# Kernel optimization log

Measured on AMD Instinct MI355X. Metric: run time of the kernel, lower is better.

Reference implementation:

```python
import jax, jax.numpy as jnp
import numpy as np

T, N, D = 64, 40, 4
H, R, K = 256, 64, 2
E = N * (N - 1)


def _xavier(key, shape):
    std = (2.0 / (shape[0] + shape[1])) ** 0.5
    return (std * jax.random.normal(key, shape)).astype(jnp.float32)


def setup_inputs() -> dict:
    ks = iter(jax.random.split(jax.random.key(0), 40))
    send, recv = np.where(np.ones((N, N)) - np.eye(N))  # fully-connected directed graph, E = N*(N-1)
    p = {}
    p['inputs'] = jax.random.normal(next(ks), (1, T, N, D), dtype=jnp.float32)
    p['node_masks'] = jnp.ones((1, T, N), dtype=jnp.float32)
    p['send_edges'] = jnp.asarray(send, dtype=jnp.int32)
    p['recv_edges'] = jnp.asarray(recv, dtype=jnp.int32)
    for name, nin in (('mlp1', D), ('mlp2', 2 * H), ('mlp3', H), ('mlp4', 3 * H)):
        p[name + '_W1'] = _xavier(next(ks), (H, nin))
        p[name + '_b1'] = jnp.full((H,), 0.1, jnp.float32)
        p[name + '_W2'] = _xavier(next(ks), (H, H))
        p[name + '_b2'] = jnp.full((H,), 0.1, jnp.float32)
    s = float(1.0 / np.sqrt(R))
    for nm in ('fwd', 'rev'):
        p[nm + '_Wih'] = jax.random.uniform(next(ks), (4 * R, H), jnp.float32, -s, s)
        p[nm + '_Whh'] = jax.random.uniform(next(ks), (4 * R, R), jnp.float32, -s, s)
        p[nm + '_bih'] = jnp.zeros((4 * R,), jnp.float32)
        p[nm + '_bhh'] = jnp.zeros((4 * R,), jnp.float32)
    p['enc_W'] = _xavier(next(ks), (K, 2 * R))
    p['enc_b'] = jnp.full((K,), 0.1, jnp.float32)
    p['prior_W'] = _xavier(next(ks), (K, R))
    p['prior_b'] = jnp.full((K,), 0.1, jnp.float32)
    return p


def _mlp(x, W1, b1, W2, b2):
    # RefNRIMLP in eval mode with no_bn=True: elu(fc2(elu(fc1(x))))
    return jax.nn.elu(jax.nn.elu(x @ W1.T + b1) @ W2.T + b2)


def _lstm(xs, Wih, Whh, bih, bhh):
    # xs: [T, E, H] -> hidden states [T, E, R]; PyTorch LSTM gate order i, f, g, o
    def step(carry, xt):
        h, c = carry
        g = xt @ Wih.T + bih + h @ Whh.T + bhh
        i, f, gg, o = jnp.split(g, 4, axis=-1)
        c = jax.nn.sigmoid(f) * c + jax.nn.sigmoid(i) * jnp.tanh(gg)
        h = jax.nn.sigmoid(o) * jnp.tanh(c)
        return (h, c), h
    Rh = Whh.shape[1]
    init = (jnp.zeros((xs.shape[1], Rh), xs.dtype), jnp.zeros((xs.shape[1], Rh), xs.dtype))
    _, hs = jax.lax.scan(step, init, xs)
    return hs


def _encode(inputs, send, recv,
            m1W1, m1b1, m1W2, m1b2, m2W1, m2b1, m2W2, m2b2,
            m3W1, m3b1, m3W2, m3b2, m4W1, m4b1, m4W2, m4b2,
            fWih, fWhh, fbih, fbhh, rWih, rWhh, rbih, rbhh,
            encW, encb, priW, prib):
    x = inputs[0]                                                  # [T, N, D]
    h = _mlp(x, m1W1, m1b1, m1W2, m1b2)                            # [T, N, H]
    e = jnp.concatenate([h[:, send], h[:, recv]], axis=-1)         # node2edge gather [T, E, 2H]
    e = _mlp(e, m2W1, m2b1, m2W2, m2b2)                            # [T, E, H]
    skip = e
    n = jnp.zeros((x.shape[0], x.shape[1], e.shape[-1]), e.dtype)
    n = n.at[:, recv].add(e)                                       # edge2node scatter-add (index_add_)
    n = _mlp(n, m3W1, m3b1, m3W2, m3b2)                            # [T, N, H]
    e = jnp.concatenate([n[:, send], n[:, recv], skip], axis=-1)   # [T, E, 3H]
    e = _mlp(e, m4W1, m4b1, m4W2, m4b2)                            # per-edge features over time [T, E, H]
    fwd_h = _lstm(e, fWih, fWhh, fbih, fbhh)                       # [T, E, R]
    rev_h = _lstm(e[::-1], rWih, rWhh, rbih, rbhh)[::-1]           # [T, E, R]
    prior = fwd_h @ priW.T + prib                                  # [T, E, K]
    enc = jnp.concatenate([fwd_h, rev_h], axis=-1) @ encW.T + encb # [T, E, K]
    return jnp.concatenate([prior, enc], axis=-1)                  # [T, E, 2K]


def reference(inputs, node_masks, send_edges, recv_edges,
              mlp1_W1, mlp1_b1, mlp1_W2, mlp1_b2,
              mlp2_W1, mlp2_b1, mlp2_W2, mlp2_b2,
              mlp3_W1, mlp3_b1, mlp3_W2, mlp3_b2,
              mlp4_W1, mlp4_b1, mlp4_W2, mlp4_b2,
              fwd_Wih, fwd_Whh, fwd_bih, fwd_bhh,
              rev_Wih, rev_Whh, rev_bih, rev_bhh,
              enc_W, enc_b, prior_W, prior_b):
    del node_masks  # all nodes present -> static fully-connected graph each step
    return _encode(inputs, send_edges, recv_edges,
                   mlp1_W1, mlp1_b1, mlp1_W2, mlp1_b2,
                   mlp2_W1, mlp2_b1, mlp2_W2, mlp2_b2,
                   mlp3_W1, mlp3_b1, mlp3_W2, mlp3_b2,
                   mlp4_W1, mlp4_b1, mlp4_W2, mlp4_b2,
                   fwd_Wih, fwd_Whh, fwd_bih, fwd_bhh,
                   rev_Wih, rev_Whh, rev_bih, rev_bhh,
                   enc_W, enc_b, prior_W, prior_b)
```

## Files before the change

### kernel.cpp

```cpp
#include <hip/hip_runtime.h>
#include <math.h>

#define T_ 64
#define N_ 40
#define D_ 4
#define H_ 256
#define R_ 64
#define E_ 1560
#define TE_ (T_*E_)
#define TN_ (T_*N_)

typedef unsigned short us;
typedef short short8 __attribute__((ext_vector_type(8)));
typedef float f32x4 __attribute__((ext_vector_type(4)));

__device__ __forceinline__ float elu_f(float x){ return x > 0.f ? x : (__expf(x) - 1.f); }
__device__ __forceinline__ float sig_f(float x){ return 1.f/(1.f+__expf(-x)); }
__device__ __forceinline__ float tanh_f(float x){ return 2.f/(1.f+__expf(-2.f*x)) - 1.f; }
__device__ __forceinline__ float dot4(float4 a, float4 b){ return a.x*b.x + a.y*b.y + a.z*b.z + a.w*b.w; }

__device__ __forceinline__ float bf2f(us u){ return __uint_as_float(((unsigned int)u) << 16); }
__device__ __forceinline__ us f2bf(float f){
    unsigned int u = __float_as_uint(f);
    u += 0x7FFFu + ((u >> 16) & 1u);
    return (us)(u >> 16);
}
__device__ __forceinline__ float4 ld4f(const float* p){ return *(const float4*)p; }
__device__ __forceinline__ float4 ld4f(const us* p){
    ushort4 v = *(const ushort4*)p;
    return make_float4(bf2f(v.x), bf2f(v.y), bf2f(v.z), bf2f(v.w));
}
__device__ __forceinline__ void st4f(float* p, float4 v){ *(float4*)p = v; }
__device__ __forceinline__ void st4f(us* p, float4 v){
    ushort4 o; o.x = f2bf(v.x); o.y = f2bf(v.y); o.z = f2bf(v.z); o.w = f2bf(v.w);
    *(ushort4*)p = o;
}

__device__ __forceinline__ void gld16(void* lds, const void* g){
    __builtin_amdgcn_global_load_lds((const __attribute__((address_space(1))) unsigned int*)g,
                                     (__attribute__((address_space(3))) unsigned int*)lds,
                                     16, 0, 0);
}

__device__ __forceinline__ void wsplit1(const float* W, us* hi, us* lo, int i){
    const float w = W[i];
    const us h = f2bf(w);
    hi[i] = h;
    lo[i] = f2bf(w - bf2f(h));
}

__device__ __forceinline__ void wsplitF(const float* __restrict__ W, int stride, int colOff,
                                        us* hi, us* lo, int i){
    const int jj   = i & 7;
    const int lane = (i >> 3) & 63;
    const int mt   = (i >> 9) & 1;
    const int k    = (i >> 10) & 7;
    const int fh   = i >> 13;
    const int R = fh * 32 + mt * 16 + (lane & 15);
    const int K = k * 32 + (lane >> 4) * 8 + jj;
    const float w = W[(size_t)R * stride + colOff + K];
    const us h = f2bf(w);
    hi[i] = h;
    lo[i] = f2bf(w - bf2f(h));
}

__global__ __launch_bounds__(256)
void wsplit_all(const float* __restrict__ s0, us* h0, us* l0,
                const float* __restrict__ s1, us* h1, us* l1,
                const float* __restrict__ s2, us* h2, us* l2,
                const float* __restrict__ s3, us* h3, us* l3,
                const float* __restrict__ s4, us* h4, us* l4,
                const float* __restrict__ s5, us* h5, us* l5,
                const float* __restrict__ s6, us* h6, us* l6)
{
    int i = blockIdx.x * 256 + threadIdx.x;
    if (i < 65536) { wsplitF(s0, 256,   0, h0, l0, i); return; } i -= 65536;
    if (i < 65536) { wsplitF(s1, 768, 512, h1, l1, i); return; } i -= 65536;
    if (i < 65536) { wsplitF(s2, 256,   0, h2, l2, i); return; } i -= 65536;
    if (i < 65536) { wsplitF(s3, 256,   0, h3, l3, i); return; } i -= 65536;
    if (i < 65536) { wsplitF(s4, 256,   0, h4, l4, i); return; } i -= 65536;
    if (i < 16384) { wsplit1(s5, h5, l5, i); return; } i -= 16384;
    wsplit1(s6, h6, l6, i);
}

__global__ __launch_bounds__(256)
void mlp1_kernel(const float* __restrict__ x,
                 const float* __restrict__ W1, const float* __restrict__ b1,
                 const float* __restrict__ W2, const float* __restrict__ b2,
                 us* __restrict__ hout)
{
    __shared__ float xs[8][4];
    __shared__ float h1[8][256];
    const int tid = threadIdx.x;
    const int r0  = blockIdx.x * 8;

    if (tid < 32) xs[tid >> 2][tid & 3] = x[r0 * 4 + tid];
    __syncthreads();

    const float4 w1 = *(const float4*)&W1[tid * 4];
    const float bb1 = b1[tid];
    #pragma unroll
    for (int row = 0; row < 8; ++row) {
        float v = bb1 + xs[row][0]*w1.x + xs[row][1]*w1.y + xs[row][2]*w1.z + xs[row][3]*w1.w;
        h1[row][tid] = elu_f(v);
    }
    __syncthreads();

    float acc[8];
    const float bb2 = b2[tid];
    #pragma unroll
    for (int row = 0; row < 8; ++row) acc[row] = bb2;
    const float* w2row = W2 + (size_t)tid * 256;
    for (int k4 = 0; k4 < 64; ++k4) {
        const float4 w = *(const float4*)&w2row[k4 * 4];
        #pragma unroll
        for (int row = 0; row < 8; ++row) {
            const float4 hh = *(const float4*)&h1[row][k4 * 4];
            acc[row] += dot4(hh, w);
        }
    }
    #pragma unroll
    for (int row = 0; row < 8; ++row)
        hout[(size_t)(r0 + row) * 256 + tid] = f2bf(elu_f(acc[row]));
}

__global__ __launch_bounds__(256)
void node_proj(const us* __restrict__ A, const float* __restrict__ W,
               int wstride, float* __restrict__ P)
{
    __shared__ float As[16][64];
    __shared__ float Ws[16][64];

    const int tid  = threadIdx.x;
    const int am   = tid >> 2;
    const int gm   = blockIdx.x * 64 + am;
    const int part = blockIdx.y >> 2;
    const int wq   = blockIdx.y & 3;

    const us* aptr = A + (size_t)gm * 256;
    const float* wptr = W + (size_t)(wq * 64 + am) * wstride + part * 256;

    const int tx = tid & 15, ty = tid >> 4;
    float acc[4][4] = {};

    for (int k0 = 0; k0 < 256; k0 += 16) {
        const float4 a4 = ld4f(aptr + k0 + (tid & 3) * 4);
        const float4 w4 = *(const float4*)(wptr + k0 + (tid & 3) * 4);

        __syncthreads();
        const int ak = (tid & 3) * 4;
        As[ak+0][am] = a4.x; As[ak+1][am] = a4.y; As[ak+2][am] = a4.z; As[ak+3][am] = a4.w;
        Ws[ak+0][am] = w4.x; Ws[ak+1][am] = w4.y; Ws[ak+2][am] = w4.z; Ws[ak+3][am] = w4.w;
        __syncthreads();

        #pragma unroll
        for (int kq = 0; kq < 16; ++kq) {
            const float4 av = *(const float4*)&As[kq][ty * 4];
            const float4 wv = *(const float4*)&Ws[kq][tx * 4];
            const float a_[4] = {av.x, av.y, av.z, av.w};
            const float w_[4] = {wv.x, wv.y, wv.z, wv.w};
            #pragma unroll
            for (int i = 0; i < 4; ++i)
                #pragma unroll
                for (int j = 0; j < 4; ++j)
                    acc[i][j] += a_[i] * w_[j];
        }
    }

    const int gn = part * 256 + wq * 64 + tx * 4;
    #pragma unroll
    for (int i = 0; i < 4; ++i) {
        const int row = blockIdx.x * 64 + ty * 4 + i;
        float4 o;
        o.x = acc[i][0]; o.y = acc[i][1]; o.z = acc[i][2]; o.w = acc[i][3];
        *(float4*)(P + (size_t)row * 512 + gn) = o;
    }
}

#define VM0   0x3F70

#define GEMM_CORE64(WHp, WLp)                                                            \
    {                                                                                    \
        const us* wbh = (WHp) + w * 8192 + lane * 8;                                     \
        const us* wbl = (WLp) + w * 8192 + lane * 8;                                     \
        _Pragma("unroll")                                                                \
        for (int k = 0; k < 8; ++k) {                                                    \
            short8 wh[2], wl[2], ef[4];                                                  \
            _Pragma("unroll")                                                            \
            for (int mt = 0; mt < 2; ++mt) {                                             \
                wh[mt] = *(const short8*)(wbh + (k * 2 + mt) * 512);                     \
                wl[mt] = *(const short8*)(wbl + (k * 2 + mt) * 512);                     \
            }                                                                            \
            _Pragma("unroll")                                                            \
            for (int nt = 0; nt < 4; ++nt)                                               \
                ef[nt] = *(const short8*)(AG + k * 4096 + nt * 1024 + ml * 64 + qs16);   \
            __builtin_amdgcn_s_setprio(1);                                               \
            _Pragma("unroll")                                                            \
            for (int nt = 0; nt < 4; ++nt)                                               \
                _Pragma("unroll")                                                        \
                for (int mt = 0; mt < 2; ++mt) {                                         \
                    acc[mt][nt] = __builtin_amdgcn_mfma_f32_16x16x32_bf16(               \
                        wh[mt], ef[nt], acc[mt][nt], 0, 0, 0);                           \
                    acc[mt][nt] = __builtin_amdgcn_mfma_f32_16x16x32_bf16(               \
                        wl[mt], ef[nt], acc[mt][nt], 0, 0, 0);                           \
                }                                                                        \
            __builtin_amdgcn_s_setprio(0);                                               \
        }                                                                                \
    }

__global__ __launch_bounds__(512, 4)
void gemm_bf(const float* __restrict__ Ptab, const float* __restrict__ b1,
             const int* __restrict__ send, const int* __restrict__ recv,
             const us* __restrict__ WH, const us* __restrict__ WL,
             const float* __restrict__ bias2, us* __restrict__ C)
{
    __shared__ char AG[32768];

    const int tid = threadIdx.x, lane = tid & 63, w = tid >> 6;
    const int ml = lane & 15, q = lane >> 4;
    const int qs16 = (q ^ ((ml >> 1) & 3)) * 16;
    const int bx = blockIdx.x;

    {
        int srw[4], rrw[4];
        #pragma unroll
        for (int nt = 0; nt < 4; ++nt) {
            const int row = bx * 64 + nt * 16 + ml;
            const int t = row / E_;
            const int e = row - t * E_;
            srw[nt] = t * N_ + send[e];
            rrw[nt] = t * N_ + recv[e];
        }
        #pragma unroll
        for (int mt = 0; mt < 2; ++mt) {
            const int col = w * 32 + mt * 16 + q * 4;
            const float4 bb = *(const float4*)(b1 + col);
            const int of = w * 4096 + ml * 64 + (((mt * 2 + (q >> 1)) ^ ((ml >> 1) & 3)) * 16) + (q & 1) * 8;
            #pragma unroll
            for (int nt = 0; nt < 4; ++nt) {
                const float4 a = *(const float4*)(Ptab + (size_t)srw[nt] * 512 + col);
                const float4 b = *(const float4*)(Ptab + (size_t)rrw[nt] * 512 + 256 + col);
                float4 v;
                v.x = elu_f(a.x + b.x + bb.x);
                v.y = elu_f(a.y + b.y + bb.y);
                v.z = elu_f(a.z + b.z + bb.z);
                v.w = elu_f(a.w + b.w + bb.w);
                ushort4 o; o.x = f2bf(v.x); o.y = f2bf(v.y); o.z = f2bf(v.z); o.w = f2bf(v.w);
                *(ushort4*)(AG + of + nt * 1024) = o;
            }
        }
    }
    __syncthreads();

    f32x4 acc[2][4];
    #pragma unroll
    for (int mt = 0; mt < 2; ++mt)
        #pragma unroll
        for (int nt = 0; nt < 4; ++nt) acc[mt][nt] = (f32x4){0.f,0.f,0.f,0.f};

    GEMM_CORE64(WH, WL)

    #pragma unroll
    for (int mt = 0; mt < 2; ++mt) {
        const int col = w * 32 + mt * 16 + q * 4;
        const float4 bb = *(const float4*)(bias2 + col);
        #pragma unroll
        for (int nt = 0; nt < 4; ++nt) {
            const int row = bx * 64 + nt * 16 + ml;
            float4 v;
            v.x = elu_f(acc[mt][nt][0] + bb.x); v.y = elu_f(acc[mt][nt][1] + bb.y);
            v.z = elu_f(acc[mt][nt][2] + bb.z); v.w = elu_f(acc[mt][nt][3] + bb.w);
            ushort4 o; o.x = f2bf(v.x); o.y = f2bf(v.y); o.z = f2bf(v.z); o.w = f2bf(v.w);
            *(ushort4*)(C + (size_t)row * 256 + col) = o;
        }
    }
}

__global__ __launch_bounds__(512, 4)
void fused_m4(const us* __restrict__ Askip,
              const us* __restrict__ w4aH, const us* __restrict__ w4aL, const float* __restrict__ m4b1,
              const us* __restrict__ w4bH, const us* __restrict__ w4bL, const float* __restrict__ m4b2,
              const us* __restrict__ wfiH, const us* __restrict__ wfiL,
              const float* __restrict__ fbih, const float* __restrict__ fbhh,
              const us* __restrict__ wriH, const us* __restrict__ wriL,
              const float* __restrict__ rbih, const float* __restrict__ rbhh,
              const float* __restrict__ Ptab, const int* __restrict__ send, const int* __restrict__ recv,
              us* __restrict__ Gf, us* __restrict__ Gr)
{
    __shared__ char AG[32768];

    const int tid = threadIdx.x, lane = tid & 63, w = tid >> 6;
    const int ml = lane & 15, q = lane >> 4;
    const int lr = lane >> 2;
    const int cofs = (((lane & 3) ^ ((lane >> 3) & 3)) * 8);
    const int qs16 = (q ^ ((ml >> 1) & 3)) * 16;
    const int bx = blockIdx.x;

    int gtOf[2];
    #pragma unroll
    for (int mt = 0; mt < 2; ++mt)
        gtOf[mt] = w * 4096 + ml * 64 + (((mt * 2 + (q >> 1)) ^ ((ml >> 1) & 3)) * 16) + (q & 1) * 8;

    f32x4 acc[2][4];

    #pragma unroll
    for (int g = 0; g < 4; ++g)
        gld16(AG + w * 4096 + g * 1024,
              Askip + (size_t)(bx * 64 + g * 16 + lr) * 256 + w * 32 + cofs);
    __builtin_amdgcn_s_waitcnt(VM0);
    __syncthreads();

    ushort4 r16[2][4];

    #pragma unroll
    for (int mt = 0; mt < 2; ++mt)
        #pragma unroll
        for (int nt = 0; nt < 4; ++nt) acc[mt][nt] = (f32x4){0.f,0.f,0.f,0.f};
    GEMM_CORE64(w4aH, w4aL)
    {
        int srw[4], rrw[4];
        #pragma unroll
        for (int nt = 0; nt < 4; ++nt) {
            const int row = bx * 64 + nt * 16 + ml;
            const int t = row / E_;
            const int e = row - t * E_;
            srw[nt] = t * N_ + send[e];
            rrw[nt] = t * N_ + recv[e];
        }
        #pragma unroll
        for (int mt = 0; mt < 2; ++mt) {
            const int col = w * 32 + mt * 16 + q * 4;
            const float4 bb = *(const float4*)(m4b1 + col);
            #pragma unroll
            for (int nt = 0; nt < 4; ++nt) {
                float4 v;
                v.x = acc[mt][nt][0] + bb.x; v.y = acc[mt][nt][1] + bb.y;
                v.z = acc[mt][nt][2] + bb.z; v.w = acc[mt][nt][3] + bb.w;
                const float4 pS = *(const float4*)(Ptab + (size_t)srw[nt] * 512 + col);
                const float4 pR = *(const float4*)(Ptab + (size_t)rrw[nt] * 512 + 256 + col);
                v.x += pS.x + pR.x; v.y += pS.y + pR.y;
                v.z += pS.z + pR.z; v.w += pS.w + pR.w;
                v.x = elu_f(v.x); v.y = elu_f(v.y); v.z = elu_f(v.z); v.w = elu_f(v.w);
                ushort4 o; o.x = f2bf(v.x); o.y = f2bf(v.y); o.z = f2bf(v.z); o.w = f2bf(v.w);
                r16[mt][nt] = o;
            }
        }
    }
    __syncthreads();
    #pragma unroll
    for (int mt = 0; mt < 2; ++mt)
        #pragma unroll
        for (int nt = 0; nt < 4; ++nt)
            *(ushort4*)(AG + gtOf[mt] + nt * 1024) = r16[mt][nt];
    __syncthreads();

    #pragma unroll
    for (int mt = 0; mt < 2; ++mt)
        #pragma unroll
        for (int nt = 0; nt < 4; ++nt) acc[mt][nt] = (f32x4){0.f,0.f,0.f,0.f};
    GEMM_CORE64(w4bH, w4bL)
    #pragma unroll
    for (int mt = 0; mt < 2; ++mt) {
        const int col = w * 32 + mt * 16 + q * 4;
        const float4 bb = *(const float4*)(m4b2 + col);
        #pragma unroll
        for (int nt = 0; nt < 4; ++nt) {
            float4 v;
            v.x = elu_f(acc[mt][nt][0] + bb.x); v.y = elu_f(acc[mt][nt][1] + bb.y);
            v.z = elu_f(acc[mt][nt][2] + bb.z); v.w = elu_f(acc[mt][nt][3] + bb.w);
            ushort4 o; o.x = f2bf(v.x); o.y = f2bf(v.y); o.z = f2bf(v.z); o.w = f2bf(v.w);
            r16[mt][nt] = o;
        }
    }
    __syncthreads();
    #pragma unroll
    for (int mt = 0; mt < 2; ++mt)
        #pragma unroll
        for (int nt = 0; nt < 4; ++nt)
            *(ushort4*)(AG + gtOf[mt] + nt * 1024) = r16[mt][nt];
    __syncthreads();

    #pragma unroll
    for (int mt = 0; mt < 2; ++mt)
        #pragma unroll
        for (int nt = 0; nt < 4; ++nt) acc[mt][nt] = (f32x4){0.f,0.f,0.f,0.f};
    GEMM_CORE64(wfiH, wfiL)
    #pragma unroll
    for (int mt = 0; mt < 2; ++mt) {
        const int col = w * 32 + mt * 16 + q * 4;
        float4 bb = *(const float4*)(fbih + col);
        const float4 b2 = *(const float4*)(fbhh + col);
        bb.x += b2.x; bb.y += b2.y; bb.z += b2.z; bb.w += b2.w;
        #pragma unroll
        for (int nt = 0; nt < 4; ++nt) {
            const int row = bx * 64 + nt * 16 + ml;
            float4 v;
            v.x = acc[mt][nt][0] + bb.x; v.y = acc[mt][nt][1] + bb.y;
            v.z = acc[mt][nt][2] + bb.z; v.w = acc[mt][nt][3] + bb.w;
            ushort4 o; o.x = f2bf(v.x); o.y = f2bf(v.y); o.z = f2bf(v.z); o.w = f2bf(v.w);
            *(ushort4*)(Gf + (size_t)row * 256 + col) = o;
        }
    }

    #pragma unroll
    for (int mt = 0; mt < 2; ++mt)
        #pragma unroll
        for (int nt = 0; nt < 4; ++nt) acc[mt][nt] = (f32x4){0.f,0.f,0.f,0.f};
    GEMM_CORE64(wriH, wriL)
    #pragma unroll
    for (int mt = 0; mt < 2; ++mt) {
        const int col = w * 32 + mt * 16 + q * 4;
        float4 bb = *(const float4*)(rbih + col);
        const float4 b2 = *(const float4*)(rbhh + col);
        bb.x += b2.x; bb.y += b2.y; bb.z += b2.z; bb.w += b2.w;
        #pragma unroll
        for (int nt = 0; nt < 4; ++nt) {
            const int row = bx * 64 + nt * 16 + ml;
            float4 v;
            v.x = acc[mt][nt][0] + bb.x; v.y = acc[mt][nt][1] + bb.y;
            v.z = acc[mt][nt][2] + bb.z; v.w = acc[mt][nt][3] + bb.w;
            ushort4 o; o.x = f2bf(v.x); o.y = f2bf(v.y); o.z = f2bf(v.z); o.w = f2bf(v.w);
            *(ushort4*)(Gr + (size_t)row * 256 + col) = o;
        }
    }
}

template<bool DOELU, typename TA, typename TC>
__global__ __launch_bounds__(256)
void gemm_nt(const TA* __restrict__ A, const float* __restrict__ W,
             const float* __restrict__ bias1,
             TC* __restrict__ C, int M, int Kdim)
{
    __shared__ float As[16][64];
    __shared__ float Ws[16][64];

    const int tid = threadIdx.x;
    const int am  = tid >> 2;
    const int ak  = (tid & 3) * 4;
    const int gm  = blockIdx.x * 64 + am;

    const TA* aptr0 = A + (size_t)gm * Kdim;
    const float* wptr = W + (size_t)(blockIdx.y * 64 + am) * Kdim;

    const int tx = tid & 15, ty = tid >> 4;
    float acc[4][4] = {};

    for (int k0 = 0; k0 < Kdim; k0 += 16) {
        const float4 a4 = ld4f(aptr0 + k0 + ak);
        const float4 w4 = *(const float4*)(wptr + k0 + (tid & 3) * 4);

        __syncthreads();
        As[ak+0][am] = a4.x; As[ak+1][am] = a4.y; As[ak+2][am] = a4.z; As[ak+3][am] = a4.w;
        const int wk = (tid & 3) * 4;
        Ws[wk+0][am] = w4.x; Ws[wk+1][am] = w4.y; Ws[wk+2][am] = w4.z; Ws[wk+3][am] = w4.w;
        __syncthreads();

        #pragma unroll
        for (int kq = 0; kq < 16; ++kq) {
            const float4 av = *(const float4*)&As[kq][ty * 4];
            const float4 wv = *(const float4*)&Ws[kq][tx * 4];
            const float a_[4] = {av.x, av.y, av.z, av.w};
            const float w_[4] = {wv.x, wv.y, wv.z, wv.w};
            #pragma unroll
            for (int i = 0; i < 4; ++i)
                #pragma unroll
                for (int j = 0; j < 4; ++j)
                    acc[i][j] += a_[i] * w_[j];
        }
    }

    const int gn = blockIdx.y * 64 + tx * 4;
    const float4 bb = *(const float4*)&bias1[gn];
    #pragma unroll
    for (int i = 0; i < 4; ++i) {
        const int row = blockIdx.x * 64 + ty * 4 + i;
        float4 o;
        o.x = acc[i][0] + bb.x; o.y = acc[i][1] + bb.y;
        o.z = acc[i][2] + bb.z; o.w = acc[i][3] + bb.w;
        if (DOELU) { o.x = elu_f(o.x); o.y = elu_f(o.y); o.z = elu_f(o.z); o.w = elu_f(o.w); }
        st4f(C + (size_t)row * 256 + gn, o);
    }
}

__global__ __launch_bounds__(256)
void aggregate_kernel(const us* __restrict__ eSkip, const int* __restrict__ recv,
                      float* __restrict__ nAgg)
{
    const int t = blockIdx.x / N_;
    const int j = blockIdx.x - t * N_;
    const int c = threadIdx.x;
    const us* basep = eSkip + (size_t)t * E_ * H_ + c;
    float acc = 0.f;
    #pragma unroll
    for (int s = 0; s < N_; ++s) {
        if (s == j) continue;
        const int e = s * (N_ - 1) + (j < s ? j : j - 1);
        acc += bf2f(basep[(size_t)e * H_]);
    }
    nAgg[(size_t)blockIdx.x * H_ + c] = acc;
}

__global__ __launch_bounds__(256)
void lstm_mfma(const us* __restrict__ Gf, const us* __restrict__ Gr,
               const us* __restrict__ fWhhH, const us* __restrict__ fWhhL,
               const us* __restrict__ rWhhH, const us* __restrict__ rWhhL,
               float* __restrict__ hsF, float* __restrict__ hsR)
{
    const int NBD = (E_ + 15) / 16;
    const bool revd = (int)blockIdx.x >= NBD;
    const int blk = revd ? (int)blockIdx.x - NBD : (int)blockIdx.x;
    const int e0 = blk * 16;
    const us* G  = revd ? Gr : Gf;
    const us* WH = revd ? rWhhH : fWhhH;
    const us* WL = revd ? rWhhL : fWhhL;
    float* hs    = revd ? hsR : hsF;

    const int tid  = threadIdx.x;
    const int lane = tid & 63;
    const int w    = tid >> 6;
    const int ml   = lane & 15;
    const int q    = lane >> 4;

    __shared__ us hHi[2][16][72];
    __shared__ us hLo[2][16][72];

    short8 wfh[4][2], wfl[4][2];
    #pragma unroll
    for (int mt = 0; mt < 4; ++mt) {
        const int row = mt * 64 + w * 16 + ml;
        #pragma unroll
        for (int ks = 0; ks < 2; ++ks) {
            wfh[mt][ks] = *(const short8*)(WH + (size_t)row * 64 + ks * 32 + q * 8);
            wfl[mt][ks] = *(const short8*)(WL + (size_t)row * 64 + ks * 32 + q * 8);
        }
    }

    for (int i = tid; i < 16 * 72; i += 256) { (&hHi[0][0][0])[i] = 0; (&hLo[0][0][0])[i] = 0; }

    const int eMF = min(e0 + ml, E_ - 1);
    const bool wr = (e0 + ml) < E_;
    const int gOfs = w * 16 + q * 4;
    float4 cst = make_float4(0.f, 0.f, 0.f, 0.f);

    ushort4 gcur[4], gnxt[4];
    {
        const int tt0 = revd ? (T_ - 1) : 0;
        const us* gp = G + ((size_t)tt0 * E_ + eMF) * 256 + gOfs;
        #pragma unroll
        for (int mt = 0; mt < 4; ++mt) gcur[mt] = *(const ushort4*)(gp + mt * 64);
    }
    __syncthreads();

    for (int s = 0; s < T_; ++s) {
        const int tt = revd ? (T_ - 1 - s) : s;
        {
            const int sn = (s + 1 < T_) ? s + 1 : s;
            const int tn = revd ? (T_ - 1 - sn) : sn;
            const us* gp = G + ((size_t)tn * E_ + eMF) * 256 + gOfs;
            #pragma unroll
            for (int mt = 0; mt < 4; ++mt) gnxt[mt] = *(const ushort4*)(gp + mt * 64);
        }
        const int rb = s & 1, wb = rb ^ 1;
        short8 bh[2], bl[2];
        #pragma unroll
        for (int ks = 0; ks < 2; ++ks) {
            bh[ks] = *(const short8*)(&hHi[rb][ml][ks * 32 + q * 8]);
            bl[ks] = *(const short8*)(&hLo[rb][ml][ks * 32 + q * 8]);
        }
        f32x4 acc[4];
        #pragma unroll
        for (int mt = 0; mt < 4; ++mt) {
            acc[mt][0] = bf2f(gcur[mt].x); acc[mt][1] = bf2f(gcur[mt].y);
            acc[mt][2] = bf2f(gcur[mt].z); acc[mt][3] = bf2f(gcur[mt].w);
            #pragma unroll
            for (int ks = 0; ks < 2; ++ks) {
                acc[mt] = __builtin_amdgcn_mfma_f32_16x16x32_bf16(wfh[mt][ks], bh[ks], acc[mt], 0, 0, 0);
                acc[mt] = __builtin_amdgcn_mfma_f32_16x16x32_bf16(wfh[mt][ks], bl[ks], acc[mt], 0, 0, 0);
                acc[mt] = __builtin_amdgcn_mfma_f32_16x16x32_bf16(wfl[mt][ks], bh[ks], acc[mt], 0, 0, 0);
            }
        }
        float4 hv;
        cst.x = sig_f(acc[1][0])*cst.x + sig_f(acc[0][0])*tanh_f(acc[2][0]); hv.x = sig_f(acc[3][0])*tanh_f(cst.x);
        cst.y = sig_f(acc[1][1])*cst.y + sig_f(acc[0][1])*tanh_f(acc[2][1]); hv.y = sig_f(acc[3][1])*tanh_f(cst.y);
        cst.z = sig_f(acc[1][2])*cst.z + sig_f(acc[0][2])*tanh_f(acc[2][2]); hv.z = sig_f(acc[3][2])*tanh_f(cst.z);
        cst.w = sig_f(acc[1][3])*cst.w + sig_f(acc[0][3])*tanh_f(acc[2][3]); hv.w = sig_f(acc[3][3])*tanh_f(cst.w);
        ushort4 hh4, hl4;
        hh4.x = f2bf(hv.x); hl4.x = f2bf(hv.x - bf2f(hh4.x));
        hh4.y = f2bf(hv.y); hl4.y = f2bf(hv.y - bf2f(hh4.y));
        hh4.z = f2bf(hv.z); hl4.z = f2bf(hv.z - bf2f(hh4.z));
        hh4.w = f2bf(hv.w); hl4.w = f2bf(hv.w - bf2f(hh4.w));
        *(ushort4*)(&hHi[wb][ml][gOfs]) = hh4;
        *(ushort4*)(&hLo[wb][ml][gOfs]) = hl4;
        if (wr)
            *(float4*)(&hs[((size_t)tt * E_ + e0 + ml) * 64 + gOfs]) = hv;
        __syncthreads();
        #pragma unroll
        for (int mt = 0; mt < 4; ++mt) gcur[mt] = gnxt[mt];
    }
}

__global__ __launch_bounds__(256)
void out_kernel(const float* __restrict__ hsF, const float* __restrict__ hsR,
                const float* __restrict__ priW, const float* __restrict__ prib,
                const float* __restrict__ encW, const float* __restrict__ encb,
                float* __restrict__ out)
{
    const int idx = blockIdx.x * 256 + threadIdx.x;
    const float* f = hsF + (size_t)idx * 64;
    const float* r = hsR + (size_t)idx * 64;
    float p0 = prib[0], p1 = prib[1], q0 = encb[0], q1 = encb[1];
    #pragma unroll
    for (int k4 = 0; k4 < 16; ++k4) {
        const float4 fv = *(const float4*)(f + k4 * 4);
        const float4 rv = *(const float4*)(r + k4 * 4);
        p0 += dot4(fv, *(const float4*)(priW + k4 * 4));
        p1 += dot4(fv, *(const float4*)(priW + 64 + k4 * 4));
        q0 += dot4(fv, *(const float4*)(encW + k4 * 4))
            + dot4(rv, *(const float4*)(encW + 64 + k4 * 4));
        q1 += dot4(fv, *(const float4*)(encW + 128 + k4 * 4))
            + dot4(rv, *(const float4*)(encW + 192 + k4 * 4));
    }
    float4 o; o.x = p0; o.y = p1; o.z = q0; o.w = q1;
    *(float4*)(out + (size_t)idx * 4) = o;
}

extern "C" void kernel_launch(void* const* d_in, const int* in_sizes, int n_in,
                              void* d_out, int out_size, void* d_ws, size_t ws_size,
                              hipStream_t stream)
{
    const float* x    = (const float*)d_in[0];
    const int*   send = (const int*)d_in[2];
    const int*   recv = (const int*)d_in[3];
    const float* m1W1 = (const float*)d_in[4];  const float* m1b1 = (const float*)d_in[5];
    const float* m1W2 = (const float*)d_in[6];  const float* m1b2 = (const float*)d_in[7];
    const float* m2W1 = (const float*)d_in[8];  const float* m2b1 = (const float*)d_in[9];
    const float* m2W2 = (const float*)d_in[10]; const float* m2b2 = (const float*)d_in[11];
    const float* m3W1 = (const float*)d_in[12]; const float* m3b1 = (const float*)d_in[13];
    const float* m3W2 = (const float*)d_in[14]; const float* m3b2 = (const float*)d_in[15];
    const float* m4W1 = (const float*)d_in[16]; const float* m4b1 = (const float*)d_in[17];
    const float* m4W2 = (const float*)d_in[18]; const float* m4b2 = (const float*)d_in[19];
    const float* fWih = (const float*)d_in[20]; const float* fWhh = (const float*)d_in[21];
    const float* fbih = (const float*)d_in[22]; const float* fbhh = (const float*)d_in[23];
    const float* rWih = (const float*)d_in[24]; const float* rWhh = (const float*)d_in[25];
    const float* rbih = (const float*)d_in[26]; const float* rbhh = (const float*)d_in[27];
    const float* encW = (const float*)d_in[28]; const float* encb = (const float*)d_in[29];
    const float* priW = (const float*)d_in[30]; const float* prib = (const float*)d_in[31];

    const size_t SZN  = (size_t)TN_ * H_;
    const size_t SZE  = (size_t)TE_ * H_;
    float* n_agg = (float*)d_ws;
    float* m3t   = n_agg + SZN;
    float* Ptab  = (float*)d_ws;
    us* h16      = (us*)(m3t + SZN);
    us* n3       = h16 + SZN;
    us* w2bH = n3  + SZN;          us* w2bL = w2bH + 65536;
    us* w4aH = w2bL + 65536;       us* w4aL = w4aH + 65536;
    us* w4bH = w4aL + 65536;       us* w4bL = w4bH + 65536;
    us* wfiH = w4bL + 65536;       us* wfiL = wfiH + 65536;
    us* wriH = wfiL + 65536;       us* wriL = wriH + 65536;
    us* whfH = wriL + 65536;       us* whfL = whfH + 16384;
    us* whrH = whfL + 16384;       us* whrL = whrH + 16384;
    us* bufA16 = whrL + 16384;
    us* bufB16 = bufA16 + SZE;
    us* bufC16 = bufB16 + SZE;
    float* hsF = (float*)bufC16;
    float* hsR = hsF + (size_t)TE_ * R_;
    const size_t needed = ((size_t)(bufC16 + SZE) - (size_t)d_ws);
    if (ws_size < needed) return;

    const dim3 gN(TN_ / 64, 4), gNP(TN_ / 64, 8);

    wsplit_all<<<1408, 256, 0, stream>>>(m2W2, w2bH, w2bL,
                                         m4W1, w4aH, w4aL,
                                         m4W2, w4bH, w4bL,
                                         fWih, wfiH, wfiL, rWih, wriH, wriL,
                                         fWhh, whfH, whfL, rWhh, whrH, whrL);

    mlp1_kernel<<<TN_ / 8, 256, 0, stream>>>(x, m1W1, m1b1, m1W2, m1b2, h16);
    node_proj<<<gNP, 256, 0, stream>>>(h16, m2W1, 512, Ptab);
    gemm_bf<<<TE_ / 64, 512, 0, stream>>>(Ptab, m2b1, send, recv, w2bH, w2bL, m2b2, bufB16);
    aggregate_kernel<<<TN_, 256, 0, stream>>>(bufB16, recv, n_agg);
    gemm_nt<true, float, float><<<gN, 256, 0, stream>>>(n_agg, m3W1, m3b1, m3t, TN_, 256);
    gemm_nt<true, float, us><<<gN, 256, 0, stream>>>(m3t, m3W2, m3b2, n3, TN_, 256);
    node_proj<<<gNP, 256, 0, stream>>>(n3, m4W1, 768, Ptab);
    fused_m4<<<TE_ / 64, 512, 0, stream>>>(bufB16,
                                           w4aH, w4aL, m4b1,
                                           w4bH, w4bL, m4b2,
                                           wfiH, wfiL, fbih, fbhh,
                                           wriH, wriL, rbih, rbhh,
                                           Ptab, send, recv, bufA16, bufB16);
    lstm_mfma<<<2 * ((E_ + 15) / 16), 256, 0, stream>>>(bufA16, bufB16, whfH, whfL, whrH, whrL, hsF, hsR);
    out_kernel<<<TE_ / 256, 256, 0, stream>>>(hsF, hsR, priW, prib, encW, encb, (float*)d_out);
}
```

Before: 505.3 us.

## Fuse node aggregation, mlp3 and mlp4 node projection into one MFMA kernel

Replaces the aggregate kernel, two scalar fp32 GEMMs for mlp3 and the mlp4 node projection with a single node_chain kernel. It sums incoming edges into LDS, then runs three chained bf16 MFMA GEMMs, with split hi/lo operands to keep near-fp32 accuracy, and writes the projection table directly. The weight-split prepass is extended to cover mlp3's weights and all three column blocks of mlp4_W1. This removes several launches and intermediate global round trips, and moves the node GEMMs from scalar FMA onto matrix cores. In exchange only 40 blocks run node_chain, and the 3-term MFMA adds some compute.

```diff
diff --git a/kernel.cpp b/kernel.cpp
--- a/kernel.cpp
+++ b/kernel.cpp
@@ -30,11 +30,6 @@
     ushort4 v = *(const ushort4*)p;
     return make_float4(bf2f(v.x), bf2f(v.y), bf2f(v.z), bf2f(v.w));
 }
-__device__ __forceinline__ void st4f(float* p, float4 v){ *(float4*)p = v; }
-__device__ __forceinline__ void st4f(us* p, float4 v){
-    ushort4 o; o.x = f2bf(v.x); o.y = f2bf(v.y); o.z = f2bf(v.z); o.w = f2bf(v.w);
-    *(ushort4*)p = o;
-}
 
 __device__ __forceinline__ void gld16(void* lds, const void* g){
     __builtin_amdgcn_global_load_lds((const __attribute__((address_space(1))) unsigned int*)g,
@@ -49,19 +44,19 @@
     lo[i] = f2bf(w - bf2f(h));
 }
 
-__device__ __forceinline__ void wsplitF(const float* __restrict__ W, int stride, int colOff,
-                                        us* hi, us* lo, int i){
-    const int jj   = i & 7;
-    const int lane = (i >> 3) & 63;
-    const int mt   = (i >> 9) & 1;
-    const int k    = (i >> 10) & 7;
-    const int fh   = i >> 13;
+__device__ __forceinline__ void wsplitF2(const float* __restrict__ W, int stride, int colOff,
+                                         us* hi, us* lo, int li, int di){
+    const int jj   = li & 7;
+    const int lane = (li >> 3) & 63;
+    const int mt   = (li >> 9) & 1;
+    const int k    = (li >> 10) & 7;
+    const int fh   = li >> 13;
     const int R = fh * 32 + mt * 16 + (lane & 15);
     const int K = k * 32 + (lane >> 4) * 8 + jj;
     const float w = W[(size_t)R * stride + colOff + K];
     const us h = f2bf(w);
-    hi[i] = h;
-    lo[i] = f2bf(w - bf2f(h));
+    hi[di] = h;
+    lo[di] = f2bf(w - bf2f(h));
 }
 
 __global__ __launch_bounds__(256)
@@ -71,16 +66,20 @@
                 const float* __restrict__ s3, us* h3, us* l3,
                 const float* __restrict__ s4, us* h4, us* l4,
                 const float* __restrict__ s5, us* h5, us* l5,
-                const float* __restrict__ s6, us* h6, us* l6)
+                const float* __restrict__ s6, us* h6, us* l6,
+                const float* __restrict__ s7, us* h7, us* l7,
+                const float* __restrict__ s8, us* h8, us* l8)
 {
     int i = blockIdx.x * 256 + threadIdx.x;
-    if (i < 65536) { wsplitF(s0, 256,   0, h0, l0, i); return; } i -= 65536;
-    if (i < 65536) { wsplitF(s1, 768, 512, h1, l1, i); return; } i -= 65536;
-    if (i < 65536) { wsplitF(s2, 256,   0, h2, l2, i); return; } i -= 65536;
-    if (i < 65536) { wsplitF(s3, 256,   0, h3, l3, i); return; } i -= 65536;
-    if (i < 65536) { wsplitF(s4, 256,   0, h4, l4, i); return; } i -= 65536;
-    if (i < 16384) { wsplit1(s5, h5, l5, i); return; } i -= 16384;
-    wsplit1(s6, h6, l6, i);
+    if (i < 65536)  { wsplitF2(s0, 256, 0, h0, l0, i, i); return; } i -= 65536;
+    if (i < 196608) { wsplitF2(s1, 768, (i >> 16) * 256, h1, l1, i & 65535, i); return; } i -= 196608;
+    if (i < 65536)  { wsplitF2(s2, 256, 0, h2, l2, i, i); return; } i -= 65536;
+    if (i < 65536)  { wsplitF2(s3, 256, 0, h3, l3, i, i); return; } i -= 65536;
+    if (i < 65536)  { wsplitF2(s4, 256, 0, h4, l4, i, i); return; } i -= 65536;
+    if (i < 65536)  { wsplitF2(s5, 256, 0, h5, l5, i, i); return; } i -= 65536;
+    if (i < 65536)  { wsplitF2(s6, 256, 0, h6, l6, i, i); return; } i -= 65536;
+    if (i < 16384)  { wsplit1(s7, h7, l7, i); return; } i -= 16384;
+    wsplit1(s8, h8, l8, i);
 }
 
 __global__ __launch_bounds__(256)
@@ -208,6 +207,74 @@
         }                                                                                \
     }
 
+#define NCORE2(WHp, WLp, PH)                                                             \
+    {                                                                                    \
+        const us* wbh = (WHp) + w * 8192 + lane * 8;                                     \
+        const us* wbl = (WLp) + w * 8192 + lane * 8;                                     \
+        _Pragma("unroll")                                                                \
+        for (int k = 0; k < 8; ++k) {                                                    \
+            short8 wh[2], wl[2], ef[4];                                                  \
+            _Pragma("unroll")                                                            \
+            for (int mt = 0; mt < 2; ++mt) {                                             \
+                wh[mt] = *(const short8*)(wbh + (k * 2 + mt) * 512);                     \
+                wl[mt] = *(const short8*)(wbl + (k * 2 + mt) * 512);                     \
+            }                                                                            \
+            _Pragma("unroll")                                                            \
+            for (int nt = 0; nt < 4; ++nt)                                               \
+                ef[nt] = *(const short8*)((PH) + k * 4096 + nt * 1024 + ml * 64 + qs16); \
+            __builtin_amdgcn_s_setprio(1);                                               \
+            _Pragma("unroll")                                                            \
+            for (int nt = 0; nt < 4; ++nt)                                               \
+                _Pragma("unroll")                                                        \
+                for (int mt = 0; mt < 2; ++mt) {                                         \
+                    acc[mt][nt] = __builtin_amdgcn_mfma_f32_16x16x32_bf16(               \
+                        wh[mt], ef[nt], acc[mt][nt], 0, 0, 0);                           \
+                    acc[mt][nt] = __builtin_amdgcn_mfma_f32_16x16x32_bf16(               \
+                        wl[mt], ef[nt], acc[mt][nt], 0, 0, 0);                           \
+                }                                                                        \
+            __builtin_amdgcn_s_setprio(0);                                               \
+        }                                                                                \
+    }
+
+#define NCORE3(WHp, WLp, PH, PL)                                                         \
+    {                                                                                    \
+        const us* wbh = (WHp) + w * 8192 + lane * 8;                                     \
+        const us* wbl = (WLp) + w * 8192 + lane * 8;                                     \
+        _Pragma("unroll")                                                                \
+        for (int k = 0; k < 8; ++k) {                                                    \
+            short8 wh[2], wl[2], efh[4], efl[4];                                         \
+            _Pragma("unroll")                                                            \
+            for (int mt = 0; mt < 2; ++mt) {                                             \
+                wh[mt] = *(const short8*)(wbh + (k * 2 + mt) * 512);                     \
+                wl[mt] = *(const short8*)(wbl + (k * 2 + mt) * 512);                     \
+            }                                                                            \
+            _Pragma("unroll")                                                            \
+            for (int nt = 0; nt < 4; ++nt) {                                             \
+                efh[nt] = *(const short8*)((PH) + k * 4096 + nt * 1024 + ml * 64 + qs16);\
+                efl[nt] = *(const short8*)((PL) + k * 4096 + nt * 1024 + ml * 64 + qs16);\
+            }                                                                            \
+            __builtin_amdgcn_s_setprio(1);                                               \
+            _Pragma("unroll")                                                            \
+            for (int nt = 0; nt < 4; ++nt)                                               \
+                _Pragma("unroll")                                                        \
+                for (int mt = 0; mt < 2; ++mt) {                                         \
+                    acc[mt][nt] = __builtin_amdgcn_mfma_f32_16x16x32_bf16(               \
+                        wh[mt], efh[nt], acc[mt][nt], 0, 0, 0);                          \
+                    acc[mt][nt] = __builtin_amdgcn_mfma_f32_16x16x32_bf16(               \
+                        wh[mt], efl[nt], acc[mt][nt], 0, 0, 0);                          \
+                    acc[mt][nt] = __builtin_amdgcn_mfma_f32_16x16x32_bf16(               \
+                        wl[mt], efh[nt], acc[mt][nt], 0, 0, 0);                          \
+                }                                                                        \
+            __builtin_amdgcn_s_setprio(0);                                               \
+        }                                                                                \
+    }
+
+#define ZERO_ACC                                                                         \
+    _Pragma("unroll")                                                                    \
+    for (int mt = 0; mt < 2; ++mt)                                                       \
+        _Pragma("unroll")                                                                \
+        for (int nt = 0; nt < 4; ++nt) acc[mt][nt] = (f32x4){0.f,0.f,0.f,0.f};
+
 __global__ __launch_bounds__(512, 4)
 void gemm_bf(const float* __restrict__ Ptab, const float* __restrict__ b1,
              const int* __restrict__ send, const int* __restrict__ recv,
@@ -253,11 +320,7 @@
     __syncthreads();
 
     f32x4 acc[2][4];
-    #pragma unroll
-    for (int mt = 0; mt < 2; ++mt)
-        #pragma unroll
-        for (int nt = 0; nt < 4; ++nt) acc[mt][nt] = (f32x4){0.f,0.f,0.f,0.f};
-
+    ZERO_ACC
     GEMM_CORE64(WH, WL)
 
     #pragma unroll
@@ -272,6 +335,140 @@
             v.z = elu_f(acc[mt][nt][2] + bb.z); v.w = elu_f(acc[mt][nt][3] + bb.w);
             ushort4 o; o.x = f2bf(v.x); o.y = f2bf(v.y); o.z = f2bf(v.z); o.w = f2bf(v.w);
             *(ushort4*)(C + (size_t)row * 256 + col) = o;
+        }
+    }
+}
+
+__global__ __launch_bounds__(512, 4)
+void node_chain(const us* __restrict__ m2out,
+                const us* __restrict__ m3aH, const us* __restrict__ m3aL, const float* __restrict__ b31,
+                const us* __restrict__ m3bH, const us* __restrict__ m3bL, const float* __restrict__ b32,
+                const us* __restrict__ w41H, const us* __restrict__ w41L,
+                float* __restrict__ Ptab)
+{
+    __shared__ char AH[32768];
+    __shared__ char AL[32768];
+
+    const int tid = threadIdx.x, lane = tid & 63, w = tid >> 6;
+    const int ml = lane & 15, q = lane >> 4;
+    const int qs16 = (q ^ ((ml >> 1) & 3)) * 16;
+    const int bx = blockIdx.x;
+
+    int gtOf[2];
+    #pragma unroll
+    for (int mt = 0; mt < 2; ++mt)
+        gtOf[mt] = w * 4096 + ml * 64 + (((mt * 2 + (q >> 1)) ^ ((ml >> 1) & 3)) * 16) + (q & 1) * 8;
+
+    #pragma unroll
+    for (int mt = 0; mt < 2; ++mt) {
+        const int col = w * 32 + mt * 16 + q * 4;
+        #pragma unroll
+        for (int nt = 0; nt < 4; ++nt) {
+            const int n = bx * 64 + nt * 16 + ml;
+            const int t = n / N_, j = n - t * N_;
+            const us* bp = m2out + (size_t)t * E_ * H_ + col;
+            float ax = 0.f, ay = 0.f, az = 0.f, aw = 0.f;
+            #pragma unroll
+            for (int s = 0; s < N_; ++s) {
+                if (s == j) continue;
+                const int e = s * (N_ - 1) + (j < s ? j : j - 1);
+                const ushort4 v = *(const ushort4*)(bp + (size_t)e * H_);
+                ax += bf2f(v.x); ay += bf2f(v.y); az += bf2f(v.z); aw += bf2f(v.w);
+            }
+            ushort4 hh, ll;
+            hh.x = f2bf(ax); ll.x = f2bf(ax - bf2f(hh.x));
+            hh.y = f2bf(ay); ll.y = f2bf(ay - bf2f(hh.y));
+            hh.z = f2bf(az); ll.z = f2bf(az - bf2f(hh.z));
+            hh.w = f2bf(aw); ll.w = f2bf(aw - bf2f(hh.w));
+            *(ushort4*)(AH + gtOf[mt] + nt * 1024) = hh;
+            *(ushort4*)(AL + gtOf[mt] + nt * 1024) = ll;
+        }
+    }
+    __syncthreads();
+
+    f32x4 acc[2][4];
+    ushort4 rh[2][4], rl[2][4];
+
+    ZERO_ACC
+    NCORE3(m3aH, m3aL, AH, AL)
+    #pragma unroll
+    for (int mt = 0; mt < 2; ++mt) {
+        const int col = w * 32 + mt * 16 + q * 4;
+        const float4 bb = *(const float4*)(b31 + col);
+        #pragma unroll
+        for (int nt = 0; nt < 4; ++nt) {
+            float4 v;
+            v.x = elu_f(acc[mt][nt][0] + bb.x); v.y = elu_f(acc[mt][nt][1] + bb.y);
+            v.z = elu_f(acc[mt][nt][2] + bb.z); v.w = elu_f(acc[mt][nt][3] + bb.w);
+            ushort4 hh, ll;
+            hh.x = f2bf(v.x); ll.x = f2bf(v.x - bf2f(hh.x));
+            hh.y = f2bf(v.y); ll.y = f2bf(v.y - bf2f(hh.y));
+            hh.z = f2bf(v.z); ll.z = f2bf(v.z - bf2f(hh.z));
+            hh.w = f2bf(v.w); ll.w = f2bf(v.w - bf2f(hh.w));
+            rh[mt][nt] = hh; rl[mt][nt] = ll;
+        }
+    }
+    __syncthreads();
+    #pragma unroll
+    for (int mt = 0; mt < 2; ++mt)
+        #pragma unroll
+        for (int nt = 0; nt < 4; ++nt) {
+            *(ushort4*)(AH + gtOf[mt] + nt * 1024) = rh[mt][nt];
+            *(ushort4*)(AL + gtOf[mt] + nt * 1024) = rl[mt][nt];
+        }
+    __syncthreads();
+
+    ZERO_ACC
+    NCORE3(m3bH, m3bL, AH, AL)
+    #pragma unroll
+    for (int mt = 0; mt < 2; ++mt) {
+        const int col = w * 32 + mt * 16 + q * 4;
+        const float4 bb = *(const float4*)(b32 + col);
+        #pragma unroll
+        for (int nt = 0; nt < 4; ++nt) {
+            ushort4 hh;
+            hh.x = f2bf(elu_f(acc[mt][nt][0] + bb.x));
+            hh.y = f2bf(elu_f(acc[mt][nt][1] + bb.y));
+            hh.z = f2bf(elu_f(acc[mt][nt][2] + bb.z));
+            hh.w = f2bf(elu_f(acc[mt][nt][3] + bb.w));
+            rh[mt][nt] = hh;
+        }
+    }
+    __syncthreads();
+    #pragma unroll
+    for (int mt = 0; mt < 2; ++mt)
+        #pragma unroll
+        for (int nt = 0; nt < 4; ++nt)
+            *(ushort4*)(AH + gtOf[mt] + nt * 1024) = rh[mt][nt];
+    __syncthreads();
+
+    ZERO_ACC
+    NCORE2(w41H, w41L, AH)
+    #pragma unroll
+    for (int mt = 0; mt < 2; ++mt) {
+        const int col = w * 32 + mt * 16 + q * 4;
+        #pragma unroll
+        for (int nt = 0; nt < 4; ++nt) {
+            const int row = bx * 64 + nt * 16 + ml;
+            float4 o;
+            o.x = acc[mt][nt][0]; o.y = acc[mt][nt][1];
+            o.z = acc[mt][nt][2]; o.w = acc[mt][nt][3];
+            *(float4*)(Ptab + (size_t)row * 512 + col) = o;
+        }
+    }
+
+    ZERO_ACC
+    NCORE2(w41H + 65536, w41L + 65536, AH)
+    #pragma unroll
+    for (int mt = 0; mt < 2; ++mt) {
+        const int col = w * 32 + mt * 16 + q * 4;
+        #pragma unroll
+        for (int nt = 0; nt < 4; ++nt) {
+            const int row = bx * 64 + nt * 16 + ml;
+            float4 o;
+            o.x = acc[mt][nt][0]; o.y = acc[mt][nt][1];
+            o.z = acc[mt][nt][2]; o.w = acc[mt][nt][3];
+            *(float4*)(Ptab + (size_t)row * 512 + 256 + col) = o;
         }
     }
 }
@@ -312,10 +509,7 @@
 
     ushort4 r16[2][4];
 
-    #pragma unroll
-    for (int mt = 0; mt < 2; ++mt)
-        #pragma unroll
-        for (int nt = 0; nt < 4; ++nt) acc[mt][nt] = (f32x4){0.f,0.f,0.f,0.f};
+    ZERO_ACC
     GEMM_CORE64(w4aH, w4aL)
     {
         int srw[4], rrw[4];
@@ -354,10 +548,7 @@
             *(ushort4*)(AG + gtOf[mt] + nt * 1024) = r16[mt][nt];
     __syncthreads();
 
-    #pragma unroll
-    for (int mt = 0; mt < 2; ++mt)
-        #pragma unroll
-        for (int nt = 0; nt < 4; ++nt) acc[mt][nt] = (f32x4){0.f,0.f,0.f,0.f};
+    ZERO_ACC
     GEMM_CORE64(w4bH, w4bL)
     #pragma unroll
     for (int mt = 0; mt < 2; ++mt) {
@@ -380,10 +571,7 @@
             *(ushort4*)(AG + gtOf[mt] + nt * 1024) = r16[mt][nt];
     __syncthreads();
 
-    #pragma unroll
-    for (int mt = 0; mt < 2; ++mt)
-        #pragma unroll
-        for (int nt = 0; nt < 4; ++nt) acc[mt][nt] = (f32x4){0.f,0.f,0.f,0.f};
+    ZERO_ACC
     GEMM_CORE64(wfiH, wfiL)
     #pragma unroll
     for (int mt = 0; mt < 2; ++mt) {
@@ -402,10 +590,7 @@
         }
     }
 
-    #pragma unroll
-    for (int mt = 0; mt < 2; ++mt)
-        #pragma unroll
-        for (int nt = 0; nt < 4; ++nt) acc[mt][nt] = (f32x4){0.f,0.f,0.f,0.f};
+    ZERO_ACC
     GEMM_CORE64(wriH, wriL)
     #pragma unroll
     for (int mt = 0; mt < 2; ++mt) {
@@ -423,81 +608,6 @@
             *(ushort4*)(Gr + (size_t)row * 256 + col) = o;
         }
     }
-}
-
-template<bool DOELU, typename TA, typename TC>
-__global__ __launch_bounds__(256)
-void gemm_nt(const TA* __restrict__ A, const float* __restrict__ W,
-             const float* __restrict__ bias1,
-             TC* __restrict__ C, int M, int Kdim)
-{
-    __shared__ float As[16][64];
-    __shared__ float Ws[16][64];
-
-    const int tid = threadIdx.x;
-    const int am  = tid >> 2;
-    const int ak  = (tid & 3) * 4;
-    const int gm  = blockIdx.x * 64 + am;
-
-    const TA* aptr0 = A + (size_t)gm * Kdim;
-    const float* wptr = W + (size_t)(blockIdx.y * 64 + am) * Kdim;
-
-    const int tx = tid & 15, ty = tid >> 4;
-    float acc[4][4] = {};
-
-    for (int k0 = 0; k0 < Kdim; k0 += 16) {
-        const float4 a4 = ld4f(aptr0 + k0 + ak);
-        const float4 w4 = *(const float4*)(wptr + k0 + (tid & 3) * 4);
-
-        __syncthreads();
-        As[ak+0][am] = a4.x; As[ak+1][am] = a4.y; As[ak+2][am] = a4.z; As[ak+3][am] = a4.w;
-        const int wk = (tid & 3) * 4;
-        Ws[wk+0][am] = w4.x; Ws[wk+1][am] = w4.y; Ws[wk+2][am] = w4.z; Ws[wk+3][am] = w4.w;
-        __syncthreads();
-
-        #pragma unroll
-        for (int kq = 0; kq < 16; ++kq) {
-            const float4 av = *(const float4*)&As[kq][ty * 4];
-            const float4 wv = *(const float4*)&Ws[kq][tx * 4];
-            const float a_[4] = {av.x, av.y, av.z, av.w};
-            const float w_[4] = {wv.x, wv.y, wv.z, wv.w};
-            #pragma unroll
-            for (int i = 0; i < 4; ++i)
-                #pragma unroll
-                for (int j = 0; j < 4; ++j)
-                    acc[i][j] += a_[i] * w_[j];
-        }
-    }
-
-    const int gn = blockIdx.y * 64 + tx * 4;
-    const float4 bb = *(const float4*)&bias1[gn];
-    #pragma unroll
-    for (int i = 0; i < 4; ++i) {
-        const int row = blockIdx.x * 64 + ty * 4 + i;
-        float4 o;
-        o.x = acc[i][0] + bb.x; o.y = acc[i][1] + bb.y;
-        o.z = acc[i][2] + bb.z; o.w = acc[i][3] + bb.w;
-        if (DOELU) { o.x = elu_f(o.x); o.y = elu_f(o.y); o.z = elu_f(o.z); o.w = elu_f(o.w); }
-        st4f(C + (size_t)row * 256 + gn, o);
-    }
-}
-
-__global__ __launch_bounds__(256)
-void aggregate_kernel(const us* __restrict__ eSkip, const int* __restrict__ recv,
-                      float* __restrict__ nAgg)
-{
-    const int t = blockIdx.x / N_;
-    const int j = blockIdx.x - t * N_;
-    const int c = threadIdx.x;
-    const us* basep = eSkip + (size_t)t * E_ * H_ + c;
-    float acc = 0.f;
-    #pragma unroll
-    for (int s = 0; s < N_; ++s) {
-        if (s == j) continue;
-        const int e = s * (N_ - 1) + (j < s ? j : j - 1);
-        acc += bf2f(basep[(size_t)e * H_]);
-    }
-    nAgg[(size_t)blockIdx.x * H_ + c] = acc;
 }
 
 __global__ __launch_bounds__(256)
@@ -648,18 +758,17 @@
 
     const size_t SZN  = (size_t)TN_ * H_;
     const size_t SZE  = (size_t)TE_ * H_;
-    float* n_agg = (float*)d_ws;
-    float* m3t   = n_agg + SZN;
-    float* Ptab  = (float*)d_ws;
-    us* h16      = (us*)(m3t + SZN);
-    us* n3       = h16 + SZN;
-    us* w2bH = n3  + SZN;          us* w2bL = w2bH + 65536;
-    us* w4aH = w2bL + 65536;       us* w4aL = w4aH + 65536;
-    us* w4bH = w4aL + 65536;       us* w4bL = w4bH + 65536;
-    us* wfiH = w4bL + 65536;       us* wfiL = wfiH + 65536;
-    us* wriH = wfiL + 65536;       us* wriL = wriH + 65536;
-    us* whfH = wriL + 65536;       us* whfL = whfH + 16384;
-    us* whrH = whfL + 16384;       us* whrL = whrH + 16384;
+    float* Ptab = (float*)d_ws;
+    us* h16     = (us*)(Ptab + (size_t)TN_ * 512);
+    us* w2bH = h16  + SZN;          us* w2bL = w2bH + 65536;
+    us* w41H = w2bL + 65536;        us* w41L = w41H + 196608;
+    us* w4bH = w41L + 196608;       us* w4bL = w4bH + 65536;
+    us* wfiH = w4bL + 65536;        us* wfiL = wfiH + 65536;
+    us* wriH = wfiL + 65536;        us* wriL = wriH + 65536;
+    us* m3aH = wriL + 65536;        us* m3aL = m3aH + 65536;
+    us* m3bH = m3aL + 65536;        us* m3bL = m3bH + 65536;
+    us* whfH = m3bL + 65536;        us* whfL = whfH + 16384;
+    us* whrH = whfL + 16384;        us* whrL = whrH + 16384;
     us* bufA16 = whrL + 16384;
     us* bufB16 = bufA16 + SZE;
     us* bufC16 = bufB16 + SZE;
@@ -668,23 +777,22 @@
     const size_t needed = ((size_t)(bufC16 + SZE) - (size_t)d_ws);
     if (ws_size < needed) return;
 
-    const dim3 gN(TN_ / 64, 4), gNP(TN_ / 64, 8);
-
-    wsplit_all<<<1408, 256, 0, stream>>>(m2W2, w2bH, w2bL,
-                                         m4W1, w4aH, w4aL,
+    const dim3 gNP(TN_ / 64, 8);
+
+    wsplit_all<<<2432, 256, 0, stream>>>(m2W2, w2bH, w2bL,
+                                         m4W1, w41H, w41L,
                                          m4W2, w4bH, w4bL,
                                          fWih, wfiH, wfiL, rWih, wriH, wriL,
+                                         m3W1, m3aH, m3aL, m3W2, m3bH, m3bL,
                                          fWhh, whfH, whfL, rWhh, whrH, whrL);
 
     mlp1_kernel<<<TN_ / 8, 256, 0, stream>>>(x, m1W1, m1b1, m1W2, m1b2, h16);
     node_proj<<<gNP, 256, 0, stream>>>(h16, m2W1, 512, Ptab);
     gemm_bf<<<TE_ / 64, 512, 0, stream>>>(Ptab, m2b1, send, recv, w2bH, w2bL, m2b2, bufB16);
-    aggregate_kernel<<<TN_, 256, 0, stream>>>(bufB16, recv, n_agg);
-    gemm_nt<true, float, float><<<gN, 256, 0, stream>>>(n_agg, m3W1, m3b1, m3t, TN_, 256);
-    gemm_nt<true, float, us><<<gN, 256, 0, stream>>>(m3t, m3W2, m3b2, n3, TN_, 256);
-    node_proj<<<gNP, 256, 0, stream>>>(n3, m4W1, 768, Ptab);
+    node_chain<<<TN_ / 64, 512, 0, stream>>>(bufB16, m3aH, m3aL, m3b1, m3bH, m3bL, m3b2,
+                                             w41H, w41L, Ptab);
     fused_m4<<<TE_ / 64, 512, 0, stream>>>(bufB16,
-                                           w4aH, w4aL, m4b1,
+                                           w41H + 131072, w41L + 131072, m4b1,
                                            w4bH, w4bL, m4b2,
                                            wfiH, wfiL, fbih, fbhh,
                                            wriH, wriL, rbih, rbhh,
```

New measurement: 577.0 us. +14.2%, slower.
